# Optimization experiments

Measured on AMD Instinct MI355X. Metric: run time of the kernel, lower is better.

Reference implementation:

```python
import jax, jax.numpy as jnp
import numpy as np

D = 512  # c_size == q_size


def setup_inputs() -> dict:
    key = jax.random.key(0)
    ks = jax.random.split(key, 8)
    c = jax.random.normal(ks[0], (8, 2048, D), dtype=jnp.float32)
    q = jax.random.normal(ks[1], (8, 512, D), dtype=jnp.float32)
    sc = 1.0 / np.sqrt(D)
    w_c = jax.random.uniform(ks[2], (D,), jnp.float32, -sc, sc)
    b_c = jax.random.uniform(ks[3], (), jnp.float32, -sc, sc)
    w_q = jax.random.uniform(ks[4], (D,), jnp.float32, -sc, sc)
    b_q = jax.random.uniform(ks[5], (), jnp.float32, -sc, sc)
    w_cq = jax.random.uniform(ks[6], (D,), jnp.float32, -sc, sc)
    b_cq = jax.random.uniform(ks[7], (), jnp.float32, -sc, sc)
    return {"c": c, "q": q, "w_c": w_c, "b_c": b_c, "w_q": w_q, "b_q": b_q,
            "w_cq": w_cq, "b_cq": b_cq}


def reference(c, q, w_c, b_c, w_q, b_q, w_cq, b_cq):
    # s[b,t,i] = <c[b,t],w_c>+b_c + <q[b,i],w_q>+b_q + <c[b,t]*q[b,i], w_cq>+b_cq
    # The original per-query-token loop for att_weight_cq(c*qi) collapses to
    # a single batched contraction since the Linear is linear in c*qi.
    sc = jnp.einsum('btd,d->bt', c, w_c) + b_c          # (B, c_len)
    sq = jnp.einsum('bid,d->bi', q, w_q) + b_q          # (B, q_len)
    scq = jnp.einsum('btd,bid->bti', c * w_cq, q) + b_cq  # (B, c_len, q_len)
    s = sc[:, :, None] + sq[:, None, :] + scq

    a = jax.nn.softmax(s, axis=2)                       # attend over q
    c2q = jnp.einsum('bti,bid->btd', a, q)              # (B, c_len, D)

    b = jax.nn.softmax(jnp.max(s, axis=2), axis=1)      # (B, c_len)
    q2c = jnp.einsum('bt,btd->bd', b, c)                # (B, D)
    q2c = jnp.broadcast_to(q2c[:, None, :], c.shape)    # (B, c_len, D)

    x = jnp.concatenate([c, c2q, c * c2q, c * q2c], axis=-1)
    return x
```

## Files before the change

### kernel.cpp

```cpp
#include <hip/hip_runtime.h>
#include <cstdint>


constexpr int kB = 8;
constexpr int kT = 2048;
constexpr int kI = 512;
constexpr int kD = 512;
constexpr int kW = 4 * kD;
constexpr int kRows = 64;
constexpr int kTiles = kT / kRows;
constexpr int kChunk = kRows * 72;

using f32x4  = __attribute__((ext_vector_type(4))) float;
using bf16x4 = __attribute__((ext_vector_type(4))) __bf16;
using bf16x8 = __attribute__((ext_vector_type(8))) __bf16;

__device__ __forceinline__ float dot8(const f32x4& a0, const f32x4& a1,
                                      const f32x4& b0, const f32x4& b1) {
  return a0.x * b0.x + a0.y * b0.y + a0.z * b0.z + a0.w * b0.w +
         a1.x * b1.x + a1.y * b1.y + a1.z * b1.z + a1.w * b1.w;
}

__global__ __launch_bounds__(256) void prep_kernel(
    const float* __restrict__ q, const float* __restrict__ w_q,
    const float* __restrict__ b_q, float* __restrict__ sq,
    __bf16* __restrict__ qf, __bf16* __restrict__ vf) {
  const int b = blockIdx.y;
  const int tid = threadIdx.x;
  if (blockIdx.x < 32) {
    __shared__ float sacc[16][17];
    const int g = blockIdx.x;
    const int kk0 = tid >> 6;
    const int lane = tid & 63;
    const int lr = lane & 15, lg = lane >> 4;
    const float* row = q + ((size_t)(b * kI + g * 16 + lr)) * kD;
    float sp = 0.f;
#pragma unroll
    for (int kk = kk0; kk < 16; kk += 4) {
      const int ka = kk * 32 + lg * 8;
      f32x4 v0 = *(const f32x4*)(row + ka);
      f32x4 v1 = *(const f32x4*)(row + ka + 4);
      f32x4 u0 = *(const f32x4*)(w_q + ka);
      f32x4 u1 = *(const f32x4*)(w_q + ka + 4);
      sp += dot8(v0, v1, u0, u1);
      bf16x8 o = {(__bf16)v0.x, (__bf16)v0.y, (__bf16)v0.z, (__bf16)v0.w,
                  (__bf16)v1.x, (__bf16)v1.y, (__bf16)v1.z, (__bf16)v1.w};
      *(bf16x8*)(qf + ((((size_t)(b * 32 + g)) * 16 + kk) << 9) + lane * 8) = o;
    }
    sacc[lr][kk0 * 4 + lg] = sp;
    __syncthreads();
    if (tid < 16) {
      float s = 0.f;
#pragma unroll
      for (int j = 0; j < 16; ++j) s += sacc[tid][j];
      sq[b * kI + g * 16 + tid] = s + b_q[0];
    }
  } else {
    __shared__ float ts[64][68];
    const int blk = blockIdx.x - 32;
    const int i0 = (blk & 7) * 64;
    const int d0 = (blk >> 3) * 64;
    const int r = tid >> 2;
    const int cg = (tid & 3) * 16;
#pragma unroll
    for (int j = 0; j < 4; ++j) {
      f32x4 v = *(const f32x4*)(q + ((size_t)(b * kI + i0 + r)) * kD + d0 + cg + 4 * j);
      ts[r][cg + 4 * j + 0] = v.x;
      ts[r][cg + 4 * j + 1] = v.y;
      ts[r][cg + 4 * j + 2] = v.z;
      ts[r][cg + 4 * j + 3] = v.w;
    }
    __syncthreads();
    const int dl = tid >> 2;
    const int ig = (tid & 3) * 16;
    bf16x8 o0, o1;
#pragma unroll
    for (int j = 0; j < 8; ++j) o0[j] = (__bf16)ts[ig + j][dl];
#pragma unroll
    for (int j = 0; j < 8; ++j) o1[j] = (__bf16)ts[ig + 8 + j][dl];
    const int gd = (d0 >> 4) + (dl >> 4);
    const int lr = dl & 15;
    const int kki0 = (i0 >> 5) + (ig >> 5);
    const int lg0 = (ig & 31) >> 3;
    const int i1 = ig + 8;
    const int kki1 = (i0 >> 5) + (i1 >> 5);
    const int lg1 = (i1 & 31) >> 3;
    *(bf16x8*)(vf + ((((size_t)(b * 32 + gd)) * 16 + kki0) << 9) +
               (lg0 * 16 + lr) * 8) = o0;
    *(bf16x8*)(vf + ((((size_t)(b * 32 + gd)) * 16 + kki1) << 9) +
               (lg1 * 16 + lr) * 8) = o1;
  }
}

__global__ __launch_bounds__(512, 2) void fused_attn(
    const float* __restrict__ c, const __bf16* __restrict__ qf,
    const __bf16* __restrict__ vf, const float* __restrict__ w_cq,
    const float* __restrict__ w_c, const float* __restrict__ b_c,
    const float* __restrict__ b_cq, const float* __restrict__ sq,
    float* __restrict__ out, float* __restrict__ mz,
    float* __restrict__ u_tile) {
  __shared__ __align__(16) char lAP[16 * kChunk];
  __shared__ float scrow[kRows];
  __shared__ float redm[8 * kRows];
  __shared__ float reds[8 * kRows];

  const int b = blockIdx.y;
  const int tile = blockIdx.x;
  const int t0 = tile * kRows;
  const int tid = threadIdx.x;
  const int w = tid >> 6;
  const int lane = tid & 63;
  const int lr = lane & 15, lg = lane >> 4;

  const __bf16* qfb = qf + (((size_t)(b * 32 + w * 4)) * 16 << 9) + lane * 8;
  bf16x8 b0[4], b1[4], b2[4], b3[4];
#pragma unroll
  for (int n4 = 0; n4 < 4; ++n4)
    b0[n4] = *(const bf16x8*)(qfb + (((size_t)(n4 * 16 + 0)) << 9));
#pragma unroll
  for (int n4 = 0; n4 < 4; ++n4)
    b1[n4] = *(const bf16x8*)(qfb + (((size_t)(n4 * 16 + 1)) << 9));
#pragma unroll
  for (int n4 = 0; n4 < 4; ++n4)
    b2[n4] = *(const bf16x8*)(qfb + (((size_t)(n4 * 16 + 2)) << 9));

  {
    const int srow = tid >> 3;
    const int col4 = (tid & 7) * 4;
    const float* crow = c + ((size_t)(b * kT + t0 + srow)) * kD;
    float* orow0 = out + ((size_t)(b * kT + t0 + srow)) * kW;
    float scp = 0.f;
#pragma unroll
    for (int j = 0; j < 16; ++j) {
      const int col = col4 + j * 32;
      f32x4 v = *(const f32x4*)(crow + col);
      *(f32x4*)(orow0 + col) = v;
      const f32x4 wq = *(const f32x4*)(w_cq + col);
      const f32x4 wc = *(const f32x4*)(w_c + col);
      scp += v.x * wc.x + v.y * wc.y + v.z * wc.z + v.w * wc.w;
      v *= wq;
      bf16x4 bv = {(__bf16)v.x, (__bf16)v.y, (__bf16)v.z, (__bf16)v.w};
      *(bf16x4*)(lAP + j * kChunk + srow * 72 + col4 * 2) = bv;
    }
    scp += __shfl_xor(scp, 1, 64);
    scp += __shfl_xor(scp, 2, 64);
    scp += __shfl_xor(scp, 4, 64);
    if ((tid & 7) == 0) scrow[srow] = scp + b_c[0];
  }
  __syncthreads();

  f32x4 acc[4][4] = {};
#pragma unroll
  for (int kk = 0; kk < 16; ++kk) {
    if (kk < 13) {
#pragma unroll
      for (int n4 = 0; n4 < 4; ++n4)
        b3[n4] = *(const bf16x8*)(qfb + (((size_t)(n4 * 16 + kk + 3)) << 9));
    }
    bf16x8 af[4];
#pragma unroll
    for (int m = 0; m < 4; ++m)
      af[m] = *(const bf16x8*)(lAP + kk * kChunk + (m * 16 + lr) * 72 + lg * 16);
#pragma unroll
    for (int m = 0; m < 4; ++m)
#pragma unroll
      for (int n4 = 0; n4 < 4; ++n4)
        acc[m][n4] = __builtin_amdgcn_mfma_f32_16x16x32_bf16(af[m], b0[n4],
                                                             acc[m][n4], 0, 0, 0);
#pragma unroll
    for (int n4 = 0; n4 < 4; ++n4) {
      b0[n4] = b1[n4];
      b1[n4] = b2[n4];
      b2[n4] = b3[n4];
    }
  }

  const float bq = b_cq[0];
  float sqv[4];
#pragma unroll
  for (int n4 = 0; n4 < 4; ++n4) sqv[n4] = sq[b * kI + w * 64 + n4 * 16 + lr];
  float scr[4][4];
#pragma unroll
  for (int m = 0; m < 4; ++m)
#pragma unroll
    for (int r = 0; r < 4; ++r) scr[m][r] = scrow[m * 16 + lg * 4 + r] + bq;
#pragma unroll
  for (int m = 0; m < 4; ++m)
#pragma unroll
    for (int n4 = 0; n4 < 4; ++n4)
#pragma unroll
      for (int r = 0; r < 4; ++r) acc[m][n4][r] += scr[m][r] + sqv[n4];

  float mx[4][4];
#pragma unroll
  for (int m = 0; m < 4; ++m)
#pragma unroll
    for (int r = 0; r < 4; ++r) {
      float v = acc[m][0][r];
#pragma unroll
      for (int n4 = 1; n4 < 4; ++n4) v = fmaxf(v, acc[m][n4][r]);
#pragma unroll
      for (int off = 1; off <= 8; off <<= 1) v = fmaxf(v, __shfl_xor(v, off, 64));
      mx[m][r] = v;
    }
  if (lr == 0) {
#pragma unroll
    for (int m = 0; m < 4; ++m)
#pragma unroll
      for (int r = 0; r < 4; ++r)
        redm[w * kRows + m * 16 + lg * 4 + r] = mx[m][r];
  }
  __syncthreads();
#pragma unroll
  for (int m = 0; m < 4; ++m)
#pragma unroll
    for (int r = 0; r < 4; ++r) {
      const int rw = m * 16 + lg * 4 + r;
      float v = redm[rw];
#pragma unroll
      for (int w2 = 1; w2 < 8; ++w2) v = fmaxf(v, redm[w2 * kRows + rw]);
      mx[m][r] = v;
    }

  float sm[4][4] = {};
#pragma unroll
  for (int m = 0; m < 4; ++m)
#pragma unroll
    for (int n4 = 0; n4 < 4; ++n4)
#pragma unroll
      for (int r = 0; r < 4; ++r) {
        const float p = __expf(acc[m][n4][r] - mx[m][r]);
        acc[m][n4][r] = p;
        sm[m][r] += p;
      }
#pragma unroll
  for (int m = 0; m < 4; ++m)
#pragma unroll
    for (int r = 0; r < 4; ++r)
#pragma unroll
      for (int off = 1; off <= 8; off <<= 1)
        sm[m][r] += __shfl_xor(sm[m][r], off, 64);
  if (lr == 0) {
#pragma unroll
    for (int m = 0; m < 4; ++m)
#pragma unroll
      for (int r = 0; r < 4; ++r)
        reds[w * kRows + m * 16 + lg * 4 + r] = sm[m][r];
  }
  __syncthreads();
  float inv[4][4];
#pragma unroll
  for (int m = 0; m < 4; ++m)
#pragma unroll
    for (int r = 0; r < 4; ++r) {
      const int rw = m * 16 + lg * 4 + r;
      float v = reds[rw];
#pragma unroll
      for (int w2 = 1; w2 < 8; ++w2) v += reds[w2 * kRows + rw];
      inv[m][r] = 1.f / v;
    }

  const __bf16* vfb = vf + (((size_t)(b * 32 + w * 4)) * 16 << 9) + lane * 8;
  bf16x8 v0_[4], v1_[4], v2_[4], v3_[4];
#pragma unroll
  for (int n4 = 0; n4 < 4; ++n4)
    v0_[n4] = *(const bf16x8*)(vfb + (((size_t)(n4 * 16 + 0)) << 9));
#pragma unroll
  for (int n4 = 0; n4 < 4; ++n4)
    v1_[n4] = *(const bf16x8*)(vfb + (((size_t)(n4 * 16 + 1)) << 9));
#pragma unroll
  for (int n4 = 0; n4 < 4; ++n4)
    v2_[n4] = *(const bf16x8*)(vfb + (((size_t)(n4 * 16 + 2)) << 9));

#pragma unroll
  for (int m = 0; m < 4; ++m)
#pragma unroll
    for (int r = 0; r < 4; ++r) {
      const int trow = m * 16 + lg * 4 + r;
#pragma unroll
      for (int n4 = 0; n4 < 4; ++n4) {
        const int icol = w * 64 + n4 * 16 + lr;
        const int kkc = icol >> 5, kc = icol & 31;
        *(__bf16*)(lAP + kkc * kChunk + trow * 72 + kc * 2) =
            (__bf16)(acc[m][n4][r] * inv[m][r]);
      }
    }
  __syncthreads();

  f32x4 o[4][4] = {};
#pragma unroll
  for (int kki = 0; kki < 16; ++kki) {
    if (kki < 13) {
#pragma unroll
      for (int n4 = 0; n4 < 4; ++n4)
        v3_[n4] = *(const bf16x8*)(vfb + (((size_t)(n4 * 16 + kki + 3)) << 9));
    }
    bf16x8 af[4];
#pragma unroll
    for (int m = 0; m < 4; ++m)
      af[m] = *(const bf16x8*)(lAP + kki * kChunk + (m * 16 + lr) * 72 + lg * 16);
#pragma unroll
    for (int m = 0; m < 4; ++m)
#pragma unroll
      for (int n4 = 0; n4 < 4; ++n4)
        o[m][n4] = __builtin_amdgcn_mfma_f32_16x16x32_bf16(af[m], v0_[n4],
                                                           o[m][n4], 0, 0, 0);
#pragma unroll
    for (int n4 = 0; n4 < 4; ++n4) {
      v0_[n4] = v1_[n4];
      v1_[n4] = v2_[n4];
      v2_[n4] = v3_[n4];
    }
  }

  float m_tile;
  {
    float v = mx[0][0];
#pragma unroll
    for (int m = 0; m < 4; ++m)
#pragma unroll
      for (int r = 0; r < 4; ++r) v = fmaxf(v, mx[m][r]);
    v = fmaxf(v, __shfl_xor(v, 16, 64));
    v = fmaxf(v, __shfl_xor(v, 32, 64));
    m_tile = v;
  }
  float u[4] = {};
  float zz = 0.f;
#pragma unroll
  for (int m = 0; m < 4; ++m)
#pragma unroll
    for (int r = 0; r < 4; ++r) {
      const int t = t0 + m * 16 + lg * 4 + r;
      const size_t rb = (size_t)(b * kT + t);
      float* orow = out + rb * kW;
      const float ev = __expf(mx[m][r] - m_tile);
      zz += ev;
#pragma unroll
      for (int n4 = 0; n4 < 4; ++n4) {
        const int d = w * 64 + n4 * 16 + lr;
        const float cvv = orow[d];
        const float pv = o[m][n4][r];
        orow[kD + d] = pv;
        orow[2 * kD + d] = cvv * pv;
        u[n4] += ev * cvv;
      }
    }
#pragma unroll
  for (int n4 = 0; n4 < 4; ++n4) {
    u[n4] += __shfl_xor(u[n4], 16, 64);
    u[n4] += __shfl_xor(u[n4], 32, 64);
  }
  if (lg == 0) {
    float* ub = u_tile + ((size_t)(b * kTiles + tile)) * kD;
#pragma unroll
    for (int n4 = 0; n4 < 4; ++n4) ub[w * 64 + n4 * 16 + lr] = u[n4];
  }
  if (w == 0) {
    zz += __shfl_xor(zz, 16, 64);
    zz += __shfl_xor(zz, 32, 64);
    if (lane == 0) {
      mz[b * 64 + tile] = m_tile;
      mz[b * 64 + 32 + tile] = zz;
    }
  }
}

__global__ __launch_bounds__(512) void slot3_merge_kernel(
    const float* __restrict__ mz, const float* __restrict__ u_tile,
    float* __restrict__ out) {
  const int b = blockIdx.y;
  const int tile = blockIdx.x;
  const int t0 = tile * kRows;
  const int tid = threadIdx.x;
  __shared__ float sM[32], sZ[32];
  __shared__ float sq2c[kD];
  if (tid < 32) {
    sM[tid] = mz[b * 64 + tid];
    sZ[tid] = mz[b * 64 + 32 + tid];
  }
  __syncthreads();
  {
    float M = sM[0];
#pragma unroll
    for (int k = 1; k < 32; ++k) M = fmaxf(M, sM[k]);
    float Z = 0.f;
    float s = 0.f;
#pragma unroll
    for (int k = 0; k < 32; ++k) {
      const float wk = __expf(sM[k] - M);
      Z += wk * sZ[k];
      s += wk * u_tile[((size_t)(b * kTiles + k)) * kD + tid];
    }
    sq2c[tid] = s / Z;
  }
  __syncthreads();
  const int srow = tid >> 3;
  const int col4 = (tid & 7) * 4;
  const size_t rb = (size_t)(b * kT + t0 + srow);
  float* orow = out + rb * kW;
#pragma unroll
  for (int j = 0; j < 16; ++j) {
    const int col = col4 + j * 32;
    const f32x4 cv = *(const f32x4*)(orow + col);
    const f32x4 qc = *(const f32x4*)(sq2c + col);
    *(f32x4*)(orow + 3 * kD + col) = cv * qc;
  }
}

extern "C" void kernel_launch(void* const* d_in, const int* in_sizes, int n_in,
                              void* d_out, int out_size, void* d_ws, size_t ws_size,
                              hipStream_t stream) {
  const float* c    = (const float*)d_in[0];
  const float* q    = (const float*)d_in[1];
  const float* w_c  = (const float*)d_in[2];
  const float* b_c  = (const float*)d_in[3];
  const float* w_q  = (const float*)d_in[4];
  const float* b_q  = (const float*)d_in[5];
  const float* w_cq = (const float*)d_in[6];
  const float* b_cq = (const float*)d_in[7];
  float* out = (float*)d_out;
  float* ws = (float*)d_ws;

  float* sq     = ws;
  float* mz     = sq + kB * kI;
  float* u_tile = mz + kB * 64;
  __bf16* qf = (__bf16*)(u_tile + (size_t)kB * kTiles * kD);
  __bf16* vf = qf + (size_t)kB * kI * kD;

  dim3 gp(96, kB);
  prep_kernel<<<gp, 256, 0, stream>>>(q, w_q, b_q, sq, qf, vf);

  dim3 gf(kTiles, kB);
  fused_attn<<<gf, 512, 0, stream>>>(c, qf, vf, w_cq, w_c, b_c, b_cq, sq, out,
                                     mz, u_tile);

  slot3_merge_kernel<<<gf, 512, 0, stream>>>(mz, u_tile, out);
}
```

Measured before the change: 71.21 us.

## Split PV GEMM per row group and interleave batches in 1D grid

The second (attention times V) MFMA loop is restructured to process one 16-row group at a time, so only a quarter of the output accumulator is held in registers. Each group's results are written out and folded into the q2c partial sums right away. The V fragments are reloaded from global/L2 for every row group, which trades extra loads for lower register pressure under the 2-blocks-per-SM launch bound. Separately, the grid becomes 1D with batch in the low bits, so neighbouring blocks work on different batches, which changes L2 locality and scheduling order.

Measured after the change: 81.55 us. +14.5%, slower.

```diff
diff --git a/kernel.cpp b/kernel.cpp
--- a/kernel.cpp
+++ b/kernel.cpp
@@ -104,8 +104,9 @@
   __shared__ float redm[8 * kRows];
   __shared__ float reds[8 * kRows];
 
-  const int b = blockIdx.y;
-  const int tile = blockIdx.x;
+  const int bid = blockIdx.x;
+  const int b = bid & 7;
+  const int tile = bid >> 3;
   const int t0 = tile * kRows;
   const int tid = threadIdx.x;
   const int w = tid >> 6;
@@ -260,18 +261,6 @@
       inv[m][r] = 1.f / v;
     }
 
-  const __bf16* vfb = vf + (((size_t)(b * 32 + w * 4)) * 16 << 9) + lane * 8;
-  bf16x8 v0_[4], v1_[4], v2_[4], v3_[4];
-#pragma unroll
-  for (int n4 = 0; n4 < 4; ++n4)
-    v0_[n4] = *(const bf16x8*)(vfb + (((size_t)(n4 * 16 + 0)) << 9));
-#pragma unroll
-  for (int n4 = 0; n4 < 4; ++n4)
-    v1_[n4] = *(const bf16x8*)(vfb + (((size_t)(n4 * 16 + 1)) << 9));
-#pragma unroll
-  for (int n4 = 0; n4 < 4; ++n4)
-    v2_[n4] = *(const bf16x8*)(vfb + (((size_t)(n4 * 16 + 2)) << 9));
-
 #pragma unroll
   for (int m = 0; m < 4; ++m)
 #pragma unroll
@@ -285,33 +274,6 @@
             (__bf16)(acc[m][n4][r] * inv[m][r]);
       }
     }
-  __syncthreads();
-
-  f32x4 o[4][4] = {};
-#pragma unroll
-  for (int kki = 0; kki < 16; ++kki) {
-    if (kki < 13) {
-#pragma unroll
-      for (int n4 = 0; n4 < 4; ++n4)
-        v3_[n4] = *(const bf16x8*)(vfb + (((size_t)(n4 * 16 + kki + 3)) << 9));
-    }
-    bf16x8 af[4];
-#pragma unroll
-    for (int m = 0; m < 4; ++m)
-      af[m] = *(const bf16x8*)(lAP + kki * kChunk + (m * 16 + lr) * 72 + lg * 16);
-#pragma unroll
-    for (int m = 0; m < 4; ++m)
-#pragma unroll
-      for (int n4 = 0; n4 < 4; ++n4)
-        o[m][n4] = __builtin_amdgcn_mfma_f32_16x16x32_bf16(af[m], v0_[n4],
-                                                           o[m][n4], 0, 0, 0);
-#pragma unroll
-    for (int n4 = 0; n4 < 4; ++n4) {
-      v0_[n4] = v1_[n4];
-      v1_[n4] = v2_[n4];
-      v2_[n4] = v3_[n4];
-    }
-  }
 
   float m_tile;
   {
@@ -324,27 +286,67 @@
     v = fmaxf(v, __shfl_xor(v, 32, 64));
     m_tile = v;
   }
+  float ev[4][4];
+  float zz = 0.f;
+#pragma unroll
+  for (int m = 0; m < 4; ++m)
+#pragma unroll
+    for (int r = 0; r < 4; ++r) {
+      ev[m][r] = __expf(mx[m][r] - m_tile);
+      zz += ev[m][r];
+    }
+  __syncthreads();
+
+  const __bf16* vfb = vf + (((size_t)(b * 32 + w * 4)) * 16 << 9) + lane * 8;
   float u[4] = {};
-  float zz = 0.f;
-#pragma unroll
-  for (int m = 0; m < 4; ++m)
-#pragma unroll
-    for (int r = 0; r < 4; ++r) {
-      const int t = t0 + m * 16 + lg * 4 + r;
-      const size_t rb = (size_t)(b * kT + t);
-      float* orow = out + rb * kW;
-      const float ev = __expf(mx[m][r] - m_tile);
-      zz += ev;
+#pragma unroll
+  for (int mg = 0; mg < 4; ++mg) {
+    bf16x8 v0_[4], v1_[4], v2_[4], v3_[4];
+#pragma unroll
+    for (int n4 = 0; n4 < 4; ++n4)
+      v0_[n4] = *(const bf16x8*)(vfb + (((size_t)(n4 * 16 + 0)) << 9));
+#pragma unroll
+    for (int n4 = 0; n4 < 4; ++n4)
+      v1_[n4] = *(const bf16x8*)(vfb + (((size_t)(n4 * 16 + 1)) << 9));
+#pragma unroll
+    for (int n4 = 0; n4 < 4; ++n4)
+      v2_[n4] = *(const bf16x8*)(vfb + (((size_t)(n4 * 16 + 2)) << 9));
+    f32x4 o[4] = {};
+#pragma unroll
+    for (int kki = 0; kki < 16; ++kki) {
+      if (kki < 13) {
+#pragma unroll
+        for (int n4 = 0; n4 < 4; ++n4)
+          v3_[n4] = *(const bf16x8*)(vfb + (((size_t)(n4 * 16 + kki + 3)) << 9));
+      }
+      const bf16x8 af =
+          *(const bf16x8*)(lAP + kki * kChunk + (mg * 16 + lr) * 72 + lg * 16);
+#pragma unroll
+      for (int n4 = 0; n4 < 4; ++n4)
+        o[n4] = __builtin_amdgcn_mfma_f32_16x16x32_bf16(af, v0_[n4], o[n4], 0, 0, 0);
+#pragma unroll
+      for (int n4 = 0; n4 < 4; ++n4) {
+        v0_[n4] = v1_[n4];
+        v1_[n4] = v2_[n4];
+        v2_[n4] = v3_[n4];
+      }
+    }
+#pragma unroll
+    for (int r = 0; r < 4; ++r) {
+      const int t = t0 + mg * 16 + lg * 4 + r;
+      float* orow = out + ((size_t)(b * kT + t)) * kW;
 #pragma unroll
       for (int n4 = 0; n4 < 4; ++n4) {
         const int d = w * 64 + n4 * 16 + lr;
         const float cvv = orow[d];
-        const float pv = o[m][n4][r];
+        const float pv = o[n4][r];
         orow[kD + d] = pv;
         orow[2 * kD + d] = cvv * pv;
-        u[n4] += ev * cvv;
+        u[n4] += ev[mg][r] * cvv;
       }
     }
+  }
+
 #pragma unroll
   for (int n4 = 0; n4 < 4; ++n4) {
     u[n4] += __shfl_xor(u[n4], 16, 64);
@@ -368,8 +370,9 @@
 __global__ __launch_bounds__(512) void slot3_merge_kernel(
     const float* __restrict__ mz, const float* __restrict__ u_tile,
     float* __restrict__ out) {
-  const int b = blockIdx.y;
-  const int tile = blockIdx.x;
+  const int bid = blockIdx.x;
+  const int b = bid & 7;
+  const int tile = bid >> 3;
   const int t0 = tile * kRows;
   const int tid = threadIdx.x;
   __shared__ float sM[32], sZ[32];
@@ -430,9 +433,8 @@
   dim3 gp(96, kB);
   prep_kernel<<<gp, 256, 0, stream>>>(q, w_q, b_q, sq, qf, vf);
 
-  dim3 gf(kTiles, kB);
-  fused_attn<<<gf, 512, 0, stream>>>(c, qf, vf, w_cq, w_c, b_c, b_cq, sq, out,
-                                     mz, u_tile);
-
-  slot3_merge_kernel<<<gf, 512, 0, stream>>>(mz, u_tile, out);
+  fused_attn<<<kB * kTiles, 512, 0, stream>>>(c, qf, vf, w_cq, w_c, b_c, b_cq,
+                                              sq, out, mz, u_tile);
+
+  slot3_merge_kernel<<<kB * kTiles, 512, 0, stream>>>(mz, u_tile, out);
 }
```
